# Kernel tuning notes

Hardware: AMD Instinct MI355X
Metric: run time of the kernel (lower is better)

Reference implementation:

```python
import jax, jax.numpy as jnp
import numpy as np

NUM_USERS = 200000
NUM_ITEMS = 100000
NUM_NODES = NUM_USERS + NUM_ITEMS
EMBED_DIM = 64
NUM_EDGES = 2000000
NUM_LAYERS = 2


def setup_inputs() -> dict:
    key = jax.random.key(0)
    k1, k2, k3, k4, k5 = jax.random.split(key, 5)
    u_embs = jax.random.normal(k1, (NUM_USERS, EMBED_DIM), dtype=jnp.float32)
    i_embs = jax.random.normal(k2, (NUM_ITEMS, EMBED_DIM), dtype=jnp.float32)
    edge_src = jax.random.randint(k3, (NUM_EDGES,), 0, NUM_NODES, dtype=jnp.int32)
    edge_dst = jax.random.randint(k4, (NUM_EDGES,), 0, NUM_NODES, dtype=jnp.int32)
    # precomputed symmetric-normalized adjacency weights (1/sqrt(du*di) in the original)
    edge_weight = jax.random.uniform(k5, (NUM_EDGES,), dtype=jnp.float32)
    return {
        "u_embs": u_embs,
        "i_embs": i_embs,
        "edge_src": edge_src,
        "edge_dst": edge_dst,
        "edge_weight": edge_weight,
    }


def _gcn_smooth(embs, edge_src, edge_dst, edge_weight):
    # sparse SpMM: out[d] = sum_{e: dst(e)=d} w_e * embs[src(e)]
    msgs = embs[edge_src] * edge_weight[:, None]  # [E, D]
    return jax.ops.segment_sum(msgs, edge_dst, num_segments=NUM_NODES)


def reference(u_embs, i_embs, edge_src, edge_dst, edge_weight):
    all_embs = jnp.concatenate([u_embs, i_embs], axis=0)  # [N, D]
    acc = all_embs  # running sum over layer outputs (layer 0 included)
    x = all_embs
    for _ in range(NUM_LAYERS):
        x = _gcn_smooth(x, edge_src, edge_dst, edge_weight)
        acc = acc + x
    return acc / jnp.float32(NUM_LAYERS + 1)  # mean over stacked layers
```

## Files before the change

### kernel.cpp

```cpp
#include <hip/hip_runtime.h>
#include <hip/hip_bf16.h>

#define NUSERS 200000
#define NITEMS 100000
#define NNODES 300000
#define EDIM   64
#define NEDGES 2000000
#define SCAN_NB ((NNODES + 255) / 256)
#define FILL_BLOCKS 2048
#define NPASS 4
#define PREP_HB 2048
#define PREP_CB 2048
#define SPMM_BLOCKS 2048
#define SPMM_STRIDE (SPMM_BLOCKS * 4)

typedef unsigned short u16;

__device__ __forceinline__ float bf2f(u16 h) {
    return __uint_as_float((unsigned)h << 16);
}
__device__ __forceinline__ u16 f2bf(float f) {
    union { __hip_bfloat16 b; u16 u; } c;
    c.b = __float2bfloat16(f);
    return c.u;
}

__global__ void k_prep(const int4* __restrict__ dst4, int* __restrict__ cnt,
                       const float4* __restrict__ uq, const float4* __restrict__ iq,
                       ushort4* __restrict__ xb4) {
    int b = blockIdx.x;
    if (b < PREP_HB) {
        for (int i = b * 256 + threadIdx.x; i < NEDGES / 4; i += PREP_HB * 256) {
            int4 d = dst4[i];
            atomicAdd(&cnt[d.x], 1);
            atomicAdd(&cnt[d.y], 1);
            atomicAdd(&cnt[d.z], 1);
            atomicAdd(&cnt[d.w], 1);
        }
    } else {
        for (int i = (b - PREP_HB) * 256 + threadIdx.x; i < NNODES * 16;
             i += PREP_CB * 256) {
            float4 v = (i < NUSERS * 16) ? uq[i] : iq[i - NUSERS * 16];
            ushort4 h;
            h.x = f2bf(v.x); h.y = f2bf(v.y); h.z = f2bf(v.z); h.w = f2bf(v.w);
            xb4[i] = h;
        }
    }
}


__global__ void k_scan1(int* __restrict__ data, int* __restrict__ bsum) {
    __shared__ int s[256];
    int i = blockIdx.x * 256 + threadIdx.x;
    int v = (i < NNODES) ? data[i] : 0;
    s[threadIdx.x] = v;
    __syncthreads();
    for (int o = 1; o < 256; o <<= 1) {
        int t = (threadIdx.x >= o) ? s[threadIdx.x - o] : 0;
        __syncthreads();
        s[threadIdx.x] += t;
        __syncthreads();
    }
    if (i < NNODES) data[i] = s[threadIdx.x] - v;
    if (threadIdx.x == 255) bsum[blockIdx.x] = s[255];
}

__global__ void k_scan2(int* __restrict__ bsum) {
    __shared__ int s[256];
    __shared__ int carry;
    if (threadIdx.x == 0) carry = 0;
    __syncthreads();
    for (int base = 0; base < SCAN_NB; base += 256) {
        int i = base + threadIdx.x;
        int v = (i < SCAN_NB) ? bsum[i] : 0;
        s[threadIdx.x] = v;
        __syncthreads();
        for (int o = 1; o < 256; o <<= 1) {
            int t = (threadIdx.x >= o) ? s[threadIdx.x - o] : 0;
            __syncthreads();
            s[threadIdx.x] += t;
            __syncthreads();
        }
        if (i < SCAN_NB) bsum[i] = s[threadIdx.x] - v + carry;
        __syncthreads();
        if (threadIdx.x == 0) carry += s[255];
        __syncthreads();
    }
}

__global__ void k_scan3(int* __restrict__ off, const int* __restrict__ bscan,
                        int* __restrict__ wpos) {
    int i = blockIdx.x * 256 + threadIdx.x;
    if (i < NNODES) {
        int v = off[i] + bscan[blockIdx.x];
        off[i] = v;
        wpos[i] = v;
    }
    if (i == 0) off[NNODES] = NEDGES;
}


__global__ void k_fill_win(const int* __restrict__ src, const int4* __restrict__ dst4,
                           const float* __restrict__ w, int* __restrict__ wpos,
                           int2* __restrict__ edata) {
    const int W = (NNODES + NPASS - 1) / NPASS;
    for (int k = 0; k < NPASS; ++k) {
        int lo = k * W;
        int hi = lo + W;
        for (int i = blockIdx.x * 256 + threadIdx.x; i < NEDGES / 4;
             i += FILL_BLOCKS * 256) {
            int4 d = dst4[i];
            int e = i * 4;
            if (d.x >= lo && d.x < hi) {
                int p = atomicAdd(&wpos[d.x], 1);
                edata[p] = make_int2(src[e], __float_as_int(w[e]));
            }
            if (d.y >= lo && d.y < hi) {
                int p = atomicAdd(&wpos[d.y], 1);
                edata[p] = make_int2(src[e + 1], __float_as_int(w[e + 1]));
            }
            if (d.z >= lo && d.z < hi) {
                int p = atomicAdd(&wpos[d.z], 1);
                edata[p] = make_int2(src[e + 2], __float_as_int(w[e + 2]));
            }
            if (d.w >= lo && d.w < hi) {
                int p = atomicAdd(&wpos[d.w], 1);
                edata[p] = make_int2(src[e + 3], __float_as_int(w[e + 3]));
            }
        }
    }
}


__device__ __forceinline__ float4 bfrow(const ushort4* __restrict__ xb4, int s, int l16) {
    const ushort4* p = (const ushort4*)((const char*)xb4 +
                       (((unsigned)s << 7) + ((unsigned)l16 << 3)));
    ushort4 h = *p;
    float4 v;
    v.x = bf2f(h.x); v.y = bf2f(h.y); v.z = bf2f(h.z); v.w = bf2f(h.w);
    return v;
}

__device__ __forceinline__ int2 ld_edge(const int2* __restrict__ e, int i) {
    return *(const int2*)((const char*)e + ((unsigned)i << 3));
}

__global__ __launch_bounds__(256, 8)
void k_spmm1(const ushort4* __restrict__ xb4, const int* __restrict__ off,
             const int2* __restrict__ edata, ushort4* __restrict__ x1b4) {
    const int wid  = threadIdx.x >> 6;
    const int lane = threadIdx.x & 63;
    const int q    = lane >> 4;
    const int l16  = lane & 15;
    int n = blockIdx.x * 4 + wid;
    int o0 = off[n];
    int o1 = off[n + 1];
    while (n < NNODES) {
        int nn = n + SPMM_STRIDE;
        int no0 = 0, no1 = 0;
        if (nn < NNODES) { no0 = off[nn]; no1 = off[nn + 1]; }
        int deg = o1 - o0;
        int cap = o1 - 1; if (cap < 0) cap = 0;
        int b0 = o0 + q;
        int p0 = b0;      if (p0 > cap) p0 = cap;
        int p1 = b0 + 4;  if (p1 > cap) p1 = cap;
        int p2 = b0 + 8;  if (p2 > cap) p2 = cap;
        int p3 = b0 + 12; if (p3 > cap) p3 = cap;
        int2 e0 = ld_edge(edata, p0);
        int2 e1 = ld_edge(edata, p1);
        int2 e2 = ld_edge(edata, p2);
        int2 e3 = ld_edge(edata, p3);
        float4 v0 = make_float4(0.f, 0.f, 0.f, 0.f);
        float4 v1 = v0, v2 = v0, v3 = v0;
        if (q < deg)      v0 = bfrow(xb4, e0.x, l16);
        if (q + 4 < deg)  v1 = bfrow(xb4, e1.x, l16);
        if (q + 8 < deg)  v2 = bfrow(xb4, e2.x, l16);
        if (q + 12 < deg) v3 = bfrow(xb4, e3.x, l16);
        float w0 = __int_as_float(e0.y), w1 = __int_as_float(e1.y);
        float w2 = __int_as_float(e2.y), w3 = __int_as_float(e3.y);
        float4 a0, a1;
        a0.x = w0 * v0.x; a0.y = w0 * v0.y; a0.z = w0 * v0.z; a0.w = w0 * v0.w;
        a1.x = w1 * v1.x; a1.y = w1 * v1.y; a1.z = w1 * v1.z; a1.w = w1 * v1.w;
        a0.x += w2 * v2.x; a0.y += w2 * v2.y; a0.z += w2 * v2.z; a0.w += w2 * v2.w;
        a1.x += w3 * v3.x; a1.y += w3 * v3.y; a1.z += w3 * v3.z; a1.w += w3 * v3.w;
        if (deg > 16) {
            for (int p = b0 + 16; p < o1; p += 4) {
                int2 e = ld_edge(edata, p);
                float4 v = bfrow(xb4, e.x, l16);
                float w = __int_as_float(e.y);
                a0.x += w * v.x; a0.y += w * v.y; a0.z += w * v.z; a0.w += w * v.w;
            }
        }
        a0.x += a1.x; a0.y += a1.y; a0.z += a1.z; a0.w += a1.w;
        a0.x += __shfl_xor(a0.x, 16, 64); a0.y += __shfl_xor(a0.y, 16, 64);
        a0.z += __shfl_xor(a0.z, 16, 64); a0.w += __shfl_xor(a0.w, 16, 64);
        a0.x += __shfl_xor(a0.x, 32, 64); a0.y += __shfl_xor(a0.y, 32, 64);
        a0.z += __shfl_xor(a0.z, 32, 64); a0.w += __shfl_xor(a0.w, 32, 64);
        if (q == 0) {
            ushort4 h;
            h.x = f2bf(a0.x); h.y = f2bf(a0.y); h.z = f2bf(a0.z); h.w = f2bf(a0.w);
            x1b4[(size_t)n * 16 + l16] = h;
        }
        n = nn; o0 = no0; o1 = no1;
    }
}

__global__ __launch_bounds__(256, 8)
void k_spmm2(const float4* __restrict__ uq, const float4* __restrict__ iq,
             const ushort4* __restrict__ x1b4, const int* __restrict__ off,
             const int2* __restrict__ edata, float4* __restrict__ outq) {
    const int wid  = threadIdx.x >> 6;
    const int lane = threadIdx.x & 63;
    const int q    = lane >> 4;
    const int l16  = lane & 15;
    int n = blockIdx.x * 4 + wid;
    int o0 = off[n];
    int o1 = off[n + 1];
    while (n < NNODES) {
        int nn = n + SPMM_STRIDE;
        int no0 = 0, no1 = 0;
        if (nn < NNODES) { no0 = off[nn]; no1 = off[nn + 1]; }
        int deg = o1 - o0;
        int cap = o1 - 1; if (cap < 0) cap = 0;
        int b0 = o0 + q;
        int p0 = b0;      if (p0 > cap) p0 = cap;
        int p1 = b0 + 4;  if (p1 > cap) p1 = cap;
        int p2 = b0 + 8;  if (p2 > cap) p2 = cap;
        int p3 = b0 + 12; if (p3 > cap) p3 = cap;
        int2 e0 = ld_edge(edata, p0);
        int2 e1 = ld_edge(edata, p1);
        int2 e2 = ld_edge(edata, p2);
        int2 e3 = ld_edge(edata, p3);
        float4 v0 = make_float4(0.f, 0.f, 0.f, 0.f);
        float4 v1 = v0, v2 = v0, v3 = v0;
        if (q < deg)      v0 = bfrow(x1b4, e0.x, l16);
        if (q + 4 < deg)  v1 = bfrow(x1b4, e1.x, l16);
        if (q + 8 < deg)  v2 = bfrow(x1b4, e2.x, l16);
        if (q + 12 < deg) v3 = bfrow(x1b4, e3.x, l16);
        float w0 = __int_as_float(e0.y), w1 = __int_as_float(e1.y);
        float w2 = __int_as_float(e2.y), w3 = __int_as_float(e3.y);
        float4 a0, a1;
        a0.x = w0 * v0.x; a0.y = w0 * v0.y; a0.z = w0 * v0.z; a0.w = w0 * v0.w;
        a1.x = w1 * v1.x; a1.y = w1 * v1.y; a1.z = w1 * v1.z; a1.w = w1 * v1.w;
        a0.x += w2 * v2.x; a0.y += w2 * v2.y; a0.z += w2 * v2.z; a0.w += w2 * v2.w;
        a1.x += w3 * v3.x; a1.y += w3 * v3.y; a1.z += w3 * v3.z; a1.w += w3 * v3.w;
        if (deg > 16) {
            for (int p = b0 + 16; p < o1; p += 4) {
                int2 e = ld_edge(edata, p);
                float4 v = bfrow(x1b4, e.x, l16);
                float w = __int_as_float(e.y);
                a0.x += w * v.x; a0.y += w * v.y; a0.z += w * v.z; a0.w += w * v.w;
            }
        }
        a0.x += a1.x; a0.y += a1.y; a0.z += a1.z; a0.w += a1.w;
        a0.x += __shfl_xor(a0.x, 16, 64); a0.y += __shfl_xor(a0.y, 16, 64);
        a0.z += __shfl_xor(a0.z, 16, 64); a0.w += __shfl_xor(a0.w, 16, 64);
        a0.x += __shfl_xor(a0.x, 32, 64); a0.y += __shfl_xor(a0.y, 32, 64);
        a0.z += __shfl_xor(a0.z, 32, 64); a0.w += __shfl_xor(a0.w, 32, 64);
        if (q == 0) {
            size_t ridx = (size_t)n * 16 + l16;
            float4 x0 = (n < NUSERS) ? uq[ridx] : iq[ridx - (size_t)NUSERS * 16];
            float4 x1v = bfrow(x1b4, n, l16);
            const float s = 1.0f / 3.0f;
            float4 r;
            r.x = (x0.x + x1v.x + a0.x) * s;
            r.y = (x0.y + x1v.y + a0.y) * s;
            r.z = (x0.z + x1v.z + a0.z) * s;
            r.w = (x0.w + x1v.w + a0.w) * s;
            outq[ridx] = r;
        }
        n = nn; o0 = no0; o1 = no1;
    }
}


__global__ void scatter_l1(const float* __restrict__ u, const float* __restrict__ it,
                           float* __restrict__ y,
                           const int* __restrict__ src, const int* __restrict__ dst,
                           const float* __restrict__ w) {
    long long t = (long long)blockIdx.x * blockDim.x + threadIdx.x;
    int e = (int)(t >> 4);
    if (e >= NEDGES) return;
    int q = (int)(t & 15);
    int s = src[e], d = dst[e];
    float we = w[e];
    const float* xrow = (s < NUSERS) ? (u + (size_t)s * EDIM)
                                     : (it + (size_t)(s - NUSERS) * EDIM);
    float4 v = ((const float4*)xrow)[q];
    float* yp = y + (size_t)d * EDIM + q * 4;
    atomicAdd(yp + 0, we * v.x);
    atomicAdd(yp + 1, we * v.y);
    atomicAdd(yp + 2, we * v.z);
    atomicAdd(yp + 3, we * v.w);
}

__global__ void scatter_gen(const float* __restrict__ x, float* __restrict__ y,
                            const int* __restrict__ src, const int* __restrict__ dst,
                            const float* __restrict__ w) {
    long long t = (long long)blockIdx.x * blockDim.x + threadIdx.x;
    int e = (int)(t >> 4);
    if (e >= NEDGES) return;
    int q = (int)(t & 15);
    int s = src[e], d = dst[e];
    float we = w[e];
    float4 v = ((const float4*)(x + (size_t)s * EDIM))[q];
    float* yp = y + (size_t)d * EDIM + q * 4;
    atomicAdd(yp + 0, we * v.x);
    atomicAdd(yp + 1, we * v.y);
    atomicAdd(yp + 2, we * v.z);
    atomicAdd(yp + 3, we * v.w);
}

__global__ void final_kernel(const float4* __restrict__ u, const float4* __restrict__ it,
                             const float4* __restrict__ x2, float4* __restrict__ outq) {
    int i = blockIdx.x * blockDim.x + threadIdx.x;
    const int uq = NUSERS * EDIM / 4;
    const int nq = NNODES * EDIM / 4;
    if (i >= nq) return;
    float4 x0 = (i < uq) ? u[i] : it[i - uq];
    float4 x1 = outq[i];
    float4 a  = x2[i];
    const float s = 1.0f / 3.0f;
    float4 r;
    r.x = (x0.x + x1.x + a.x) * s;
    r.y = (x0.y + x1.y + a.y) * s;
    r.z = (x0.z + x1.z + a.z) * s;
    r.w = (x0.w + x1.w + a.w) * s;
    outq[i] = r;
}


extern "C" void kernel_launch(void* const* d_in, const int* in_sizes, int n_in,
                              void* d_out, int out_size, void* d_ws, size_t ws_size,
                              hipStream_t stream) {
    const float* u   = (const float*)d_in[0];
    const float* it  = (const float*)d_in[1];
    const int*   src = (const int*)d_in[2];
    const int*   dst = (const int*)d_in[3];
    const float* w   = (const float*)d_in[4];
    float* out = (float*)d_out;

    const size_t nd = (size_t)NNODES * EDIM;

    int*     off   = (int*)d_ws;
    int*     wpos  = off + NNODES + 8;
    int*     bscan = wpos + NNODES;
    int2*    edata = (int2*)(bscan + 2048);
    ushort4* xb4   = (ushort4*)(edata + NEDGES);
    ushort4* x1b4  = xb4 + (size_t)NNODES * 16;
    const size_t needed =
        (size_t)(NNODES + 8 + NNODES + 2048) * sizeof(int) +
        (size_t)NEDGES * sizeof(int2) +
        (size_t)NNODES * 16 * sizeof(ushort4) * 2;

    dim3 blk(256);

    if (ws_size >= needed) {
        hipMemsetAsync(off, 0, (size_t)NNODES * sizeof(int), stream);
        k_prep <<<PREP_HB + PREP_CB, blk, 0, stream>>>((const int4*)dst, off,
                                              (const float4*)u, (const float4*)it, xb4);
        k_scan1<<<SCAN_NB, blk, 0, stream>>>(off, bscan);
        k_scan2<<<1, blk, 0, stream>>>(bscan);
        k_scan3<<<SCAN_NB, blk, 0, stream>>>(off, bscan, wpos);
        k_fill_win<<<FILL_BLOCKS, blk, 0, stream>>>(src, (const int4*)dst, w, wpos, edata);
        k_spmm1<<<SPMM_BLOCKS, blk, 0, stream>>>(xb4, off, edata, x1b4);
        k_spmm2<<<SPMM_BLOCKS, blk, 0, stream>>>((const float4*)u, (const float4*)it,
                                                 x1b4, off, edata, (float4*)out);
    } else {
        float* A = (float*)d_ws;
        hipMemsetAsync(out, 0, nd * sizeof(float), stream);
        long long nthreads = (long long)NEDGES * 16;
        int sblocks = (int)((nthreads + 255) / 256);
        scatter_l1<<<sblocks, blk, 0, stream>>>(u, it, out, src, dst, w);
        hipMemsetAsync(A, 0, nd * sizeof(float), stream);
        scatter_gen<<<sblocks, blk, 0, stream>>>(out, A, src, dst, w);
        final_kernel<<<(NNODES * EDIM / 4 + 255) / 256, blk, 0, stream>>>(
            (const float4*)u, (const float4*)it, (const float4*)A, (float4*)out);
    }
}
```

Before: 523.7 us.

## Replace atomic CSR build with two-level bucket sort by destination

Builds the CSR edge list with a two-level counting sort instead of per-node global atomics. Each block counts destinations into 586 shared-memory buckets of 512 nodes, and the per-block counts are scanned. Edges are then scattered into buckets, and each bucket is sorted locally in shared memory to produce offsets and edge data. This removes the global atomic contention and the four-pass windowed fill. In exchange it adds an extra edge pass and intermediate buffers, and needs a larger workspace.

```diff
diff --git a/kernel.cpp b/kernel.cpp
--- a/kernel.cpp
+++ b/kernel.cpp
@@ -6,11 +6,9 @@
 #define NNODES 300000
 #define EDIM   64
 #define NEDGES 2000000
-#define SCAN_NB ((NNODES + 255) / 256)
-#define FILL_BLOCKS 2048
-#define NPASS 4
-#define PREP_HB 2048
+#define FILLB  2048
 #define PREP_CB 2048
+#define NBKT   586
 #define SPMM_BLOCKS 2048
 #define SPMM_STRIDE (SPMM_BLOCKS * 4)
 
@@ -25,109 +23,141 @@
     return c.u;
 }
 
-__global__ void k_prep(const int4* __restrict__ dst4, int* __restrict__ cnt,
-                       const float4* __restrict__ uq, const float4* __restrict__ iq,
-                       ushort4* __restrict__ xb4) {
+
+__global__ void k_prep3(const int4* __restrict__ dst4, int* __restrict__ bc,
+                        const float4* __restrict__ uq, const float4* __restrict__ iq,
+                        ushort4* __restrict__ xb4) {
+    __shared__ int h[NBKT];
     int b = blockIdx.x;
-    if (b < PREP_HB) {
-        for (int i = b * 256 + threadIdx.x; i < NEDGES / 4; i += PREP_HB * 256) {
+    if (b < FILLB) {
+        for (int k = threadIdx.x; k < NBKT; k += 256) h[k] = 0;
+        __syncthreads();
+        for (int i = b * 256 + threadIdx.x; i < NEDGES / 4; i += FILLB * 256) {
             int4 d = dst4[i];
-            atomicAdd(&cnt[d.x], 1);
-            atomicAdd(&cnt[d.y], 1);
-            atomicAdd(&cnt[d.z], 1);
-            atomicAdd(&cnt[d.w], 1);
-        }
+            atomicAdd(&h[d.x >> 9], 1);
+            atomicAdd(&h[d.y >> 9], 1);
+            atomicAdd(&h[d.z >> 9], 1);
+            atomicAdd(&h[d.w >> 9], 1);
+        }
+        __syncthreads();
+        for (int k = threadIdx.x; k < NBKT; k += 256)
+            bc[k * FILLB + b] = h[k];
     } else {
-        for (int i = (b - PREP_HB) * 256 + threadIdx.x; i < NNODES * 16;
+        for (int i = (b - FILLB) * 256 + threadIdx.x; i < NNODES * 16;
              i += PREP_CB * 256) {
             float4 v = (i < NUSERS * 16) ? uq[i] : iq[i - NUSERS * 16];
-            ushort4 h;
-            h.x = f2bf(v.x); h.y = f2bf(v.y); h.z = f2bf(v.z); h.w = f2bf(v.w);
-            xb4[i] = h;
-        }
-    }
-}
-
-
-__global__ void k_scan1(int* __restrict__ data, int* __restrict__ bsum) {
+            ushort4 hh;
+            hh.x = f2bf(v.x); hh.y = f2bf(v.y); hh.z = f2bf(v.z); hh.w = f2bf(v.w);
+            xb4[i] = hh;
+        }
+    }
+}
+
+__global__ void k_scanb(int* __restrict__ bc, int* __restrict__ btot) {
     __shared__ int s[256];
-    int i = blockIdx.x * 256 + threadIdx.x;
-    int v = (i < NNODES) ? data[i] : 0;
-    s[threadIdx.x] = v;
+    int j = blockIdx.x;
+    int t = threadIdx.x;
+    int base = j * FILLB + t * 8;
+    int v[8];
+    int sum = 0;
+#pragma unroll
+    for (int m = 0; m < 8; ++m) { v[m] = bc[base + m]; sum += v[m]; }
+    s[t] = sum;
     __syncthreads();
     for (int o = 1; o < 256; o <<= 1) {
-        int t = (threadIdx.x >= o) ? s[threadIdx.x - o] : 0;
-        __syncthreads();
-        s[threadIdx.x] += t;
-        __syncthreads();
-    }
-    if (i < NNODES) data[i] = s[threadIdx.x] - v;
-    if (threadIdx.x == 255) bsum[blockIdx.x] = s[255];
-}
-
-__global__ void k_scan2(int* __restrict__ bsum) {
+        int x = (t >= o) ? s[t - o] : 0;
+        __syncthreads();
+        s[t] += x;
+        __syncthreads();
+    }
+    int excl = s[t] - sum;
+#pragma unroll
+    for (int m = 0; m < 8; ++m) { int x = v[m]; bc[base + m] = excl; excl += x; }
+    if (t == 255) btot[j] = s[255];
+}
+
+__global__ void k_scant(const int* __restrict__ btot, int* __restrict__ bbase,
+                        int* __restrict__ off) {
     __shared__ int s[256];
     __shared__ int carry;
-    if (threadIdx.x == 0) carry = 0;
-    __syncthreads();
-    for (int base = 0; base < SCAN_NB; base += 256) {
-        int i = base + threadIdx.x;
-        int v = (i < SCAN_NB) ? bsum[i] : 0;
-        s[threadIdx.x] = v;
+    int t = threadIdx.x;
+    if (t == 0) carry = 0;
+    __syncthreads();
+    for (int base = 0; base < NBKT; base += 256) {
+        int i = base + t;
+        int v = (i < NBKT) ? btot[i] : 0;
+        s[t] = v;
         __syncthreads();
         for (int o = 1; o < 256; o <<= 1) {
-            int t = (threadIdx.x >= o) ? s[threadIdx.x - o] : 0;
+            int x = (t >= o) ? s[t - o] : 0;
             __syncthreads();
-            s[threadIdx.x] += t;
+            s[t] += x;
             __syncthreads();
         }
-        if (i < SCAN_NB) bsum[i] = s[threadIdx.x] - v + carry;
-        __syncthreads();
-        if (threadIdx.x == 0) carry += s[255];
-        __syncthreads();
-    }
-}
-
-__global__ void k_scan3(int* __restrict__ off, const int* __restrict__ bscan,
-                        int* __restrict__ wpos) {
-    int i = blockIdx.x * 256 + threadIdx.x;
-    if (i < NNODES) {
-        int v = off[i] + bscan[blockIdx.x];
-        off[i] = v;
-        wpos[i] = v;
-    }
-    if (i == 0) off[NNODES] = NEDGES;
-}
-
-
-__global__ void k_fill_win(const int* __restrict__ src, const int4* __restrict__ dst4,
-                           const float* __restrict__ w, int* __restrict__ wpos,
-                           int2* __restrict__ edata) {
-    const int W = (NNODES + NPASS - 1) / NPASS;
-    for (int k = 0; k < NPASS; ++k) {
-        int lo = k * W;
-        int hi = lo + W;
-        for (int i = blockIdx.x * 256 + threadIdx.x; i < NEDGES / 4;
-             i += FILL_BLOCKS * 256) {
-            int4 d = dst4[i];
-            int e = i * 4;
-            if (d.x >= lo && d.x < hi) {
-                int p = atomicAdd(&wpos[d.x], 1);
-                edata[p] = make_int2(src[e], __float_as_int(w[e]));
-            }
-            if (d.y >= lo && d.y < hi) {
-                int p = atomicAdd(&wpos[d.y], 1);
-                edata[p] = make_int2(src[e + 1], __float_as_int(w[e + 1]));
-            }
-            if (d.z >= lo && d.z < hi) {
-                int p = atomicAdd(&wpos[d.z], 1);
-                edata[p] = make_int2(src[e + 2], __float_as_int(w[e + 2]));
-            }
-            if (d.w >= lo && d.w < hi) {
-                int p = atomicAdd(&wpos[d.w], 1);
-                edata[p] = make_int2(src[e + 3], __float_as_int(w[e + 3]));
-            }
-        }
+        if (i < NBKT) bbase[i] = s[t] - v + carry;
+        __syncthreads();
+        if (t == 0) carry += s[255];
+        __syncthreads();
+    }
+    if (t == 0) { bbase[NBKT] = carry; off[NNODES] = NEDGES; }
+}
+
+__global__ void k_fill3(const int4* __restrict__ dst4, const int4* __restrict__ src4,
+                        const float4* __restrict__ w4, const int* __restrict__ bc,
+                        const int* __restrict__ bbase,
+                        int* __restrict__ dstv, int2* __restrict__ sw) {
+    __shared__ int cur[NBKT];
+    int b = blockIdx.x;
+    for (int k = threadIdx.x; k < NBKT; k += 256)
+        cur[k] = bbase[k] + bc[k * FILLB + b];
+    __syncthreads();
+    for (int i = b * 256 + threadIdx.x; i < NEDGES / 4; i += FILLB * 256) {
+        int4 d = dst4[i];
+        int4 sv = src4[i];
+        float4 wv = w4[i];
+        int p;
+        p = atomicAdd(&cur[d.x >> 9], 1);
+        dstv[p] = d.x; sw[p] = make_int2(sv.x, __float_as_int(wv.x));
+        p = atomicAdd(&cur[d.y >> 9], 1);
+        dstv[p] = d.y; sw[p] = make_int2(sv.y, __float_as_int(wv.y));
+        p = atomicAdd(&cur[d.z >> 9], 1);
+        dstv[p] = d.z; sw[p] = make_int2(sv.z, __float_as_int(wv.z));
+        p = atomicAdd(&cur[d.w >> 9], 1);
+        dstv[p] = d.w; sw[p] = make_int2(sv.w, __float_as_int(wv.w));
+    }
+}
+
+__global__ void k_build(const int* __restrict__ bbase, const int* __restrict__ dstv,
+                        const int2* __restrict__ sw,
+                        int* __restrict__ off, int2* __restrict__ edata) {
+    __shared__ int cnt[512];
+    __shared__ int s[512];
+    __shared__ int cur[512];
+    int j = blockIdx.x;
+    int t = threadIdx.x;
+    int lo = bbase[j], hi = bbase[j + 1];
+    cnt[t] = 0;
+    __syncthreads();
+    for (int r = lo + t; r < hi; r += 512)
+        atomicAdd(&cnt[dstv[r] & 511], 1);
+    __syncthreads();
+    int c = cnt[t];
+    s[t] = c;
+    __syncthreads();
+    for (int o = 1; o < 512; o <<= 1) {
+        int x = (t >= o) ? s[t - o] : 0;
+        __syncthreads();
+        s[t] += x;
+        __syncthreads();
+    }
+    int excl = lo + s[t] - c;
+    cur[t] = excl;
+    int node = j * 512 + t;
+    if (node < NNODES) off[node] = excl;
+    __syncthreads();
+    for (int r = lo + t; r < hi; r += 512) {
+        int p = atomicAdd(&cur[dstv[r] & 511], 1);
+        edata[p] = sw[r];
     }
 }
 
@@ -141,8 +171,8 @@
     return v;
 }
 
-__device__ __forceinline__ int2 ld_edge(const int2* __restrict__ e, int i) {
-    return *(const int2*)((const char*)e + ((unsigned)i << 3));
+__device__ __forceinline__ int2 ld_edge(const int2* __restrict__ e, unsigned i) {
+    return *(const int2*)((const char*)e + (i << 3));
 }
 
 __global__ __launch_bounds__(256, 8)
@@ -341,28 +371,31 @@
     float* out = (float*)d_out;
 
     const size_t nd = (size_t)NNODES * EDIM;
+    dim3 blk(256);
 
     int*     off   = (int*)d_ws;
-    int*     wpos  = off + NNODES + 8;
-    int*     bscan = wpos + NNODES;
-    int2*    edata = (int2*)(bscan + 2048);
+    int*     btot  = off + NNODES + 8;
+    int*     bbase = btot + 640;
+    int*     bc    = bbase + 640;
+    int*     dstv  = bc + NBKT * FILLB;
+    int2*    sw    = (int2*)(dstv + NEDGES);
+    int2*    edata = sw + NEDGES;
     ushort4* xb4   = (ushort4*)(edata + NEDGES);
     ushort4* x1b4  = xb4 + (size_t)NNODES * 16;
-    const size_t needed =
-        (size_t)(NNODES + 8 + NNODES + 2048) * sizeof(int) +
-        (size_t)NEDGES * sizeof(int2) +
+    const size_t need_sort =
+        (size_t)(NNODES + 8 + 640 + 640 + NBKT * FILLB) * sizeof(int) +
+        (size_t)NEDGES * sizeof(int) +
+        (size_t)NEDGES * sizeof(int2) * 2 +
         (size_t)NNODES * 16 * sizeof(ushort4) * 2;
 
-    dim3 blk(256);
-
-    if (ws_size >= needed) {
-        hipMemsetAsync(off, 0, (size_t)NNODES * sizeof(int), stream);
-        k_prep <<<PREP_HB + PREP_CB, blk, 0, stream>>>((const int4*)dst, off,
-                                              (const float4*)u, (const float4*)it, xb4);
-        k_scan1<<<SCAN_NB, blk, 0, stream>>>(off, bscan);
-        k_scan2<<<1, blk, 0, stream>>>(bscan);
-        k_scan3<<<SCAN_NB, blk, 0, stream>>>(off, bscan, wpos);
-        k_fill_win<<<FILL_BLOCKS, blk, 0, stream>>>(src, (const int4*)dst, w, wpos, edata);
+    if (ws_size >= need_sort) {
+        k_prep3<<<FILLB + PREP_CB, blk, 0, stream>>>(
+            (const int4*)dst, bc, (const float4*)u, (const float4*)it, xb4);
+        k_scanb<<<NBKT, blk, 0, stream>>>(bc, btot);
+        k_scant<<<1, blk, 0, stream>>>(btot, bbase, off);
+        k_fill3<<<FILLB, blk, 0, stream>>>(
+            (const int4*)dst, (const int4*)src, (const float4*)w, bc, bbase, dstv, sw);
+        k_build<<<NBKT, dim3(512), 0, stream>>>(bbase, dstv, sw, off, edata);
         k_spmm1<<<SPMM_BLOCKS, blk, 0, stream>>>(xb4, off, edata, x1b4);
         k_spmm2<<<SPMM_BLOCKS, blk, 0, stream>>>((const float4*)u, (const float4*)it,
                                                  x1b4, off, edata, (float4*)out);
```

Measured after the change: 433.3 us. 17.3% less time.
